# Performance work log

Hardware: AMD Instinct MI355X
Metric: run time of the kernel (lower is better)

## Reference

```python
import jax, jax.numpy as jnp
import numpy as np

B, N, S, C1, C2 = 8, 8192, 2048, 128, 256
H1, H2 = 256, 256
EPS_LN = 1e-5


def _layernorm_c(x, g, b):
    # LayerNorm over channel dim of [B, C, N]
    mu = jnp.mean(x, axis=1, keepdims=True)
    var = jnp.mean((x - mu) ** 2, axis=1, keepdims=True)
    return g[None, :, None] * (x - mu) / jnp.sqrt(var + EPS_LN) + b[None, :, None]


def setup_inputs() -> dict:
    key = jax.random.key(0)
    ks = jax.random.split(key, 8)
    Cin = C1 + C2
    return {
        "points_coor1": jax.random.normal(ks[0], (B, 3, N), jnp.float32),
        "points_coor2": jax.random.normal(ks[1], (B, 3, S), jnp.float32),
        "points_fea1": jax.random.normal(ks[2], (B, C1, N), jnp.float32),
        "points_fea2": jax.random.normal(ks[3], (B, C2, S), jnp.float32),
        "points_padding2": jnp.zeros((B, S), dtype=bool),
        "W1": jax.random.normal(ks[4], (H1, Cin), jnp.float32) * 0.05,
        "b1": jnp.zeros((H1,), jnp.float32),
        "g1": jnp.ones((H1,), jnp.float32),
        "be1": jnp.zeros((H1,), jnp.float32),
        "W2": jax.random.normal(ks[5], (H2, H1), jnp.float32) * 0.05,
        "b2": jnp.zeros((H2,), jnp.float32),
        "g2": jnp.ones((H2,), jnp.float32),
        "be2": jnp.zeros((H2,), jnp.float32),
    }


def reference(points_coor1, points_coor2, points_fea1, points_fea2,
              points_padding2, W1, b1, g1, be1, W2, b2, g2, be2):
    c1 = jnp.transpose(points_coor1, (0, 2, 1))  # [B,N,3]
    c2 = jnp.transpose(points_coor2, (0, 2, 1))  # [B,S,3]
    f2 = jnp.transpose(points_fea2, (0, 2, 1))   # [B,S,C2]

    # push padded points far away (max computed on unmodified coords, as in torch RHS-first eval)
    big = jnp.max(jnp.abs(c2)) * 3.0
    c2 = jnp.where(points_padding2[..., None], big, c2)

    # squared euclidean pairwise distances [B,N,S]
    d = (jnp.sum(c1 * c1, -1)[:, :, None]
         + jnp.sum(c2 * c2, -1)[:, None, :]
         - 2.0 * jnp.einsum('bnd,bsd->bns', c1, c2))

    neg_d, idx = jax.lax.top_k(-d, 3)          # 3 smallest distances
    dists = -neg_d                              # [B,N,3]
    recip = 1.0 / jnp.clip(dists, 1e-8)
    w = recip / jnp.sum(recip, axis=-1, keepdims=True)  # [B,N,3]

    gathered = jax.vmap(lambda f, i: f[i])(f2, idx)     # [B,N,3,C2]
    interp = jnp.einsum('bnkc,bnk->bcn', gathered, w)   # [B,C2,N]

    x = jnp.concatenate([points_fea1, interp], axis=1)  # [B,C1+C2,N]
    x = jax.nn.relu(_layernorm_c(jnp.einsum('oc,bcn->bon', W1, x) + b1[None, :, None], g1, be1))
    x = jax.nn.relu(_layernorm_c(jnp.einsum('oc,bcn->bon', W2, x) + b2[None, :, None], g2, be2))
    return x
```

## Files before the change

### kernel.cpp

```cpp
#include <hip/hip_runtime.h>
#include <stdint.h>

#define BB 8
#define NPT 8192
#define SPT 2048
#define C1D 128
#define C2D 256
#define CIN 384
#define HD 256
#define SPLIT 8
#define SC (SPT/SPLIT)

typedef __attribute__((ext_vector_type(8))) short bf16x8;
typedef __attribute__((ext_vector_type(4))) float f32x4;

__device__ __forceinline__ unsigned short f2b(float f){
  unsigned int u = __float_as_uint(f);
  u += 0x7fffu + ((u >> 16) & 1u);
  return (unsigned short)(u >> 16);
}

__global__ __launch_bounds__(256) void cvt_bf16_kernel(const float* __restrict__ src,
                                                       unsigned short* __restrict__ dst, int n){
  int i = blockIdx.x * 256 + threadIdx.x;
  if (i < n) dst[i] = f2b(src[i]);
}

__global__ __launch_bounds__(256) void gsrc_kernel(const float* __restrict__ coor2,
    const unsigned char* __restrict__ pad, float4* __restrict__ gs){
  int i = blockIdx.x * 256 + threadIdx.x;
  int b = i >> 11, s = i & (SPT - 1);
  const float* cb = coor2 + b * 3 * SPT;
  float x = cb[s], y = cb[SPT + s], z = cb[2*SPT + s];
  if (pad[i]) { x = 1e19f; y = 1e19f; z = 1e19f; }
  float n2 = __fadd_rn(__fadd_rn(__fmul_rn(x,x), __fmul_rn(y,y)), __fmul_rn(z,z));
  gs[i] = make_float4(x, y, z, n2);
}

__global__ __launch_bounds__(256) void transpose_cn(const float* __restrict__ src,
    unsigned short* __restrict__ dst, int Cdim, int Ndim, int dstStride){
  __shared__ unsigned short t[32][33];
  int b = blockIdx.z;
  int n0 = blockIdx.x * 32, c0 = blockIdx.y * 32;
  int tx = threadIdx.x, ty = threadIdx.y;
  const float* s = src + (size_t)b * Cdim * Ndim;
  unsigned short* d = dst + (size_t)b * Ndim * dstStride;
  #pragma unroll
  for (int i = 0; i < 4; i++)
    t[ty + i*8][tx] = f2b(s[(size_t)(c0 + ty + i*8) * Ndim + n0 + tx]);
  __syncthreads();
  #pragma unroll
  for (int i = 0; i < 4; i++)
    d[(size_t)(n0 + ty + i*8) * dstStride + c0 + tx] = t[tx][ty + i*8];
}

__global__ __launch_bounds__(256) void knn_part_kernel(const float* __restrict__ coor1,
    const float4* __restrict__ gs, float* __restrict__ cv, int* __restrict__ cj){
  int b = blockIdx.y, c = blockIdx.z;
  int s0c = c * SC;
  const float4* gsb = gs + b * SPT + s0c;
  int n = blockIdx.x * 256 + threadIdx.x;
  const float* ca = coor1 + b * 3 * NPT;
  float x1 = ca[n], y1 = ca[NPT + n], z1 = ca[2*NPT + n];
  float n1 = __fadd_rn(__fadd_rn(__fmul_rn(x1,x1), __fmul_rn(y1,y1)), __fmul_rn(z1,z1));
  float v0 = 3.4e38f, v1 = 3.4e38f, v2 = 3.4e38f;
  int j0 = 0, j1 = 0, j2 = 0;
  #pragma unroll 8
  for (int s = 0; s < SC; s++){
    float4 q = gsb[s];
    float dot = __fadd_rn(__fadd_rn(__fmul_rn(x1,q.x), __fmul_rn(y1,q.y)), __fmul_rn(z1,q.z));
    float npn = __fadd_rn(n1, q.w);
    float d = __builtin_fmaf(-2.0f, dot, npn);
    bool l0 = d < v0, l1 = d < v1, l2 = d < v2;
    j2 = l1 ? j1 : (l2 ? s : j2);
    j1 = l0 ? j0 : (l1 ? s : j1);
    j0 = l0 ? s  : j0;
    float nv2 = __builtin_amdgcn_fmed3f(v1, v2, d);
    float nv1 = __builtin_amdgcn_fmed3f(v0, v1, d);
    v0 = fminf(v0, d); v1 = nv1; v2 = nv2;
  }
  size_t m = (size_t)b * NPT + n;
  size_t base = (m * SPLIT + c) * 3;
  cv[base+0] = v0; cv[base+1] = v1; cv[base+2] = v2;
  cj[base+0] = s0c + j0; cj[base+1] = s0c + j1; cj[base+2] = s0c + j2;
}

__global__ __launch_bounds__(256) void knn_merge_kernel(const float* __restrict__ cv,
    const int* __restrict__ cj, float* __restrict__ w3, int* __restrict__ i3){
  size_t m = (size_t)blockIdx.x * 256 + threadIdx.x;
  float v0 = 3.4e38f, v1 = 3.4e38f, v2 = 3.4e38f;
  int j0 = 0, j1 = 0, j2 = 0;
  #pragma unroll
  for (int c = 0; c < SPLIT; c++){
    #pragma unroll
    for (int k = 0; k < 3; k++){
      float d = cv[(m * SPLIT + c) * 3 + k];
      int j   = cj[(m * SPLIT + c) * 3 + k];
      bool l0 = d < v0, l1 = d < v1, l2 = d < v2;
      j2 = l1 ? j1 : (l2 ? j : j2);
      j1 = l0 ? j0 : (l1 ? j : j1);
      j0 = l0 ? j  : j0;
      float nv2 = __builtin_amdgcn_fmed3f(v1, v2, d);
      float nv1 = __builtin_amdgcn_fmed3f(v0, v1, d);
      v0 = fminf(v0, d); v1 = nv1; v2 = nv2;
    }
  }
  float r0 = 1.0f / fmaxf(v0, 1e-8f);
  float r1 = 1.0f / fmaxf(v1, 1e-8f);
  float r2 = 1.0f / fmaxf(v2, 1e-8f);
  float rs = (r0 + r1) + r2;
  w3[m*3+0] = r0 / rs; w3[m*3+1] = r1 / rs; w3[m*3+2] = r2 / rs;
  i3[m*3+0] = j0; i3[m*3+1] = j1; i3[m*3+2] = j2;
}

__global__ __launch_bounds__(256) void interp_kernel(const unsigned short* __restrict__ f2t,
    const float* __restrict__ w3, const int* __restrict__ i3, unsigned short* __restrict__ xpm){
  int m = blockIdx.x * 4 + (threadIdx.x >> 6);
  int lane = threadIdx.x & 63;
  int b = m >> 13;
  int s0 = i3[m*3+0], s1 = i3[m*3+1], s2 = i3[m*3+2];
  float w0 = w3[m*3+0], w1 = w3[m*3+1], w2 = w3[m*3+2];
  const ushort4 a = *(const ushort4*)(f2t + (size_t)(b*SPT + s0) * C2D + lane*4);
  const ushort4 c = *(const ushort4*)(f2t + (size_t)(b*SPT + s1) * C2D + lane*4);
  const ushort4 e = *(const ushort4*)(f2t + (size_t)(b*SPT + s2) * C2D + lane*4);
  #define B2F(u) __uint_as_float(((unsigned int)(u)) << 16)
  ushort4 o;
  o.x = f2b(w0*B2F(a.x) + w1*B2F(c.x) + w2*B2F(e.x));
  o.y = f2b(w0*B2F(a.y) + w1*B2F(c.y) + w2*B2F(e.y));
  o.z = f2b(w0*B2F(a.z) + w1*B2F(c.z) + w2*B2F(e.z));
  o.w = f2b(w0*B2F(a.w) + w1*B2F(c.w) + w2*B2F(e.w));
  *(ushort4*)(xpm + (size_t)m * CIN + C1D + lane*4) = o;
}

__global__ __launch_bounds__(256) void mlp1_kernel(const unsigned short* __restrict__ xpm,
    const unsigned short* __restrict__ Wg, const float* __restrict__ bg,
    const float* __restrict__ gg, const float* __restrict__ beg,
    unsigned short* __restrict__ Hg){
  __shared__ __align__(16) unsigned short Ws[256*40];
  __shared__ __align__(16) unsigned short Xs[64*40];
  __shared__ __align__(16) unsigned short Hb[64*136];
  __shared__ float sB[256], sG[256], sBe[256];
  int tid = threadIdx.x;
  int m0 = blockIdx.x * 64;
  sB[tid] = bg[tid]; sG[tid] = gg[tid]; sBe[tid] = beg[tid];
  int w = tid >> 6, lane = tid & 63, col = lane & 15, quad = lane >> 4;
  f32x4 acc[16];
  #pragma unroll
  for (int i = 0; i < 16; i++) acc[i] = (f32x4)0.0f;
  for (int kb = 0; kb < CIN; kb += 32){
    __syncthreads();
    {
      const int4* s4 = (const int4*)(Wg + (size_t)tid * CIN + kb);
      int4* d4 = (int4*)(Ws + tid * 40);
      #pragma unroll
      for (int i = 0; i < 4; i++) d4[i] = s4[i];
    }
    {
      int mr = tid >> 2, part = tid & 3;
      *(int4*)(Xs + mr*40 + part*8) = *(const int4*)(xpm + (size_t)(m0 + mr) * CIN + kb + part*8);
    }
    __syncthreads();
    bf16x8 bfrag = *(const bf16x8*)(Xs + (w*16 + col)*40 + quad*8);
    #pragma unroll
    for (int ot = 0; ot < 16; ot++){
      bf16x8 afrag = *(const bf16x8*)(Ws + (ot*16 + col)*40 + quad*8);
      acc[ot] = __builtin_amdgcn_mfma_f32_16x16x32_bf16(afrag, bfrag, acc[ot], 0, 0, 0);
    }
  }
  float s1 = 0.f, s2 = 0.f;
  #pragma unroll
  for (int ot = 0; ot < 16; ot++)
    #pragma unroll
    for (int r = 0; r < 4; r++){
      int o = ot*16 + quad*4 + r;
      float v = acc[ot][r] + sB[o];
      acc[ot][r] = v;
      s1 += v; s2 += v*v;
    }
  s1 += __shfl_xor(s1, 16); s1 += __shfl_xor(s1, 32);
  s2 += __shfl_xor(s2, 16); s2 += __shfl_xor(s2, 32);
  float mu = s1 * (1.f/256.f);
  float rinv = rsqrtf(s2 * (1.f/256.f) - mu*mu + 1e-5f);
  for (int half = 0; half < 2; half++){
    __syncthreads();
    #pragma unroll
    for (int ot8 = 0; ot8 < 8; ot8++){
      int ot = half*8 + ot8;
      int ob = ot*16 + quad*4;
      ushort4 hv;
      hv.x = f2b(fmaxf((acc[ot][0] - mu) * rinv * sG[ob+0] + sBe[ob+0], 0.f));
      hv.y = f2b(fmaxf((acc[ot][1] - mu) * rinv * sG[ob+1] + sBe[ob+1], 0.f));
      hv.z = f2b(fmaxf((acc[ot][2] - mu) * rinv * sG[ob+2] + sBe[ob+2], 0.f));
      hv.w = f2b(fmaxf((acc[ot][3] - mu) * rinv * sG[ob+3] + sBe[ob+3], 0.f));
      *(ushort4*)(Hb + (w*16 + col)*136 + ot8*16 + quad*4) = hv;
    }
    __syncthreads();
    int mr = tid >> 2, part = tid & 3;
    #pragma unroll
    for (int r = 0; r < 4; r++){
      int piece = part*4 + r;
      *(int4*)(Hg + (size_t)(m0 + mr)*HD + half*128 + piece*8) = *(const int4*)(Hb + mr*136 + piece*8);
    }
  }
}

__global__ __launch_bounds__(256) void mlp2_kernel(const unsigned short* __restrict__ Hg,
    const unsigned short* __restrict__ Wg, const float* __restrict__ bg,
    const float* __restrict__ gg, const float* __restrict__ beg,
    float* __restrict__ outg){
  __shared__ __align__(16) unsigned short Ws[256*40];
  __shared__ __align__(16) unsigned short Xs[64*40];
  __shared__ float sB[256], sG[256], sBe[256];
  int tid = threadIdx.x;
  int m0 = blockIdx.x * 64;
  int b = m0 >> 13, n0 = m0 & (NPT - 1);
  sB[tid] = bg[tid]; sG[tid] = gg[tid]; sBe[tid] = beg[tid];
  int w = tid >> 6, lane = tid & 63, col = lane & 15, quad = lane >> 4;
  f32x4 acc[16];
  #pragma unroll
  for (int i = 0; i < 16; i++) acc[i] = (f32x4)0.0f;
  for (int kb = 0; kb < HD; kb += 32){
    __syncthreads();
    {
      const int4* s4 = (const int4*)(Wg + (size_t)tid * HD + kb);
      int4* d4 = (int4*)(Ws + tid * 40);
      #pragma unroll
      for (int i = 0; i < 4; i++) d4[i] = s4[i];
    }
    {
      int mr = tid >> 2, part = tid & 3;
      *(int4*)(Xs + mr*40 + part*8) = *(const int4*)(Hg + (size_t)(m0 + mr) * HD + kb + part*8);
    }
    __syncthreads();
    bf16x8 bfrag = *(const bf16x8*)(Xs + (w*16 + col)*40 + quad*8);
    #pragma unroll
    for (int ot = 0; ot < 16; ot++){
      bf16x8 afrag = *(const bf16x8*)(Ws + (ot*16 + col)*40 + quad*8);
      acc[ot] = __builtin_amdgcn_mfma_f32_16x16x32_bf16(afrag, bfrag, acc[ot], 0, 0, 0);
    }
  }
  float s1 = 0.f, s2 = 0.f;
  #pragma unroll
  for (int ot = 0; ot < 16; ot++)
    #pragma unroll
    for (int r = 0; r < 4; r++){
      int o = ot*16 + quad*4 + r;
      float v = acc[ot][r] + sB[o];
      acc[ot][r] = v;
      s1 += v; s2 += v*v;
    }
  s1 += __shfl_xor(s1, 16); s1 += __shfl_xor(s1, 32);
  s2 += __shfl_xor(s2, 16); s2 += __shfl_xor(s2, 32);
  float mu = s1 * (1.f/256.f);
  float rinv = rsqrtf(s2 * (1.f/256.f) - mu*mu + 1e-5f);
  size_t obase = (size_t)b * HD * NPT + n0 + w*16 + col;
  #pragma unroll
  for (int ot = 0; ot < 16; ot++)
    #pragma unroll
    for (int r = 0; r < 4; r++){
      int o = ot*16 + quad*4 + r;
      float v = (acc[ot][r] - mu) * rinv * sG[o] + sBe[o];
      outg[obase + (size_t)o * NPT] = fmaxf(v, 0.f);
    }
}

extern "C" void kernel_launch(void* const* d_in, const int* in_sizes, int n_in,
                              void* d_out, int out_size, void* d_ws, size_t ws_size,
                              hipStream_t stream){
  const float* coor1 = (const float*)d_in[0];
  const float* coor2 = (const float*)d_in[1];
  const float* fea1  = (const float*)d_in[2];
  const float* fea2  = (const float*)d_in[3];
  const unsigned char* pad = (const unsigned char*)d_in[4];
  const float* W1  = (const float*)d_in[5];
  const float* b1  = (const float*)d_in[6];
  const float* g1  = (const float*)d_in[7];
  const float* be1 = (const float*)d_in[8];
  const float* W2  = (const float*)d_in[9];
  const float* b2  = (const float*)d_in[10];
  const float* g2  = (const float*)d_in[11];
  const float* be2 = (const float*)d_in[12];
  float* out = (float*)d_out;

  char* ws = (char*)d_ws;
  float* w3            = (float*)(ws + 256);
  int*   i3            = (int*)  (ws + 786688);
  unsigned short* W1b  = (unsigned short*)(ws + 1573120);
  unsigned short* W2b  = (unsigned short*)(ws + 1769728);
  unsigned short* f2t  = (unsigned short*)(ws + 1900800);
  unsigned short* xpm  = (unsigned short*)(ws + 10289408);
  unsigned short* Hg   = (unsigned short*)(ws + 60621056);
  float* cv            = (float*)(ws + 60621056);
  int*   cj            = (int*)  (ws + 60621056 + 6291456);
  float4* gs           = (float4*)(ws + 60621056 + 16777216);

  cvt_bf16_kernel<<<(HD*CIN + 255)/256, 256, 0, stream>>>(W1, W1b, HD*CIN);
  cvt_bf16_kernel<<<(HD*HD + 255)/256, 256, 0, stream>>>(W2, W2b, HD*HD);
  gsrc_kernel<<<BB*SPT/256, 256, 0, stream>>>(coor2, pad, gs);
  dim3 tb(32, 8);
  transpose_cn<<<dim3(SPT/32, C2D/32, BB), tb, 0, stream>>>(fea2, f2t, C2D, SPT, C2D);
  transpose_cn<<<dim3(NPT/32, C1D/32, BB), tb, 0, stream>>>(fea1, xpm, C1D, NPT, CIN);
  knn_part_kernel<<<dim3(NPT/256, BB, SPLIT), 256, 0, stream>>>(coor1, gs, cv, cj);
  knn_merge_kernel<<<BB*NPT/256, 256, 0, stream>>>(cv, cj, w3, i3);
  interp_kernel<<<BB*NPT/4, 256, 0, stream>>>(f2t, w3, i3, xpm);
  mlp1_kernel<<<BB*NPT/64, 256, 0, stream>>>(xpm, W1b, b1, g1, be1, Hg);
  mlp2_kernel<<<BB*NPT/64, 256, 0, stream>>>(Hg, W2b, b2, g2, be2, out);
}
```

Baseline: 287.8 us.

## Double-buffer weight tiles and prefetch activations in MLP GEMM kernels

Both MLP kernels now prefetch the next K-chunk of weights into registers and write it to a second LDS buffer while MFMAs run on the current one, cutting barriers to one per iteration. Activation fragments are loaded directly from global memory into registers rather than staged through shared memory. The two weight-to-bf16 conversion kernels are merged into one launch. This costs more LDS and registers, which may reduce occupancy.

```diff
diff --git a/kernel.cpp b/kernel.cpp
--- a/kernel.cpp
+++ b/kernel.cpp
@@ -20,10 +20,15 @@
   return (unsigned short)(u >> 16);
 }
 
-__global__ __launch_bounds__(256) void cvt_bf16_kernel(const float* __restrict__ src,
-                                                       unsigned short* __restrict__ dst, int n){
+__global__ __launch_bounds__(256) void cvt2_bf16_kernel(const float* __restrict__ W1,
+    const float* __restrict__ W2, unsigned short* __restrict__ dst){
   int i = blockIdx.x * 256 + threadIdx.x;
-  if (i < n) dst[i] = f2b(src[i]);
+  const int n1 = HD * CIN;
+  if (i < n1) dst[i] = f2b(W1[i]);
+  else {
+    int k = i - n1;
+    if (k < HD * HD) dst[n1 + k] = f2b(W2[k]);
+  }
 }
 
 __global__ __launch_bounds__(256) void gsrc_kernel(const float* __restrict__ coor2,
@@ -136,36 +141,48 @@
     const unsigned short* __restrict__ Wg, const float* __restrict__ bg,
     const float* __restrict__ gg, const float* __restrict__ beg,
     unsigned short* __restrict__ Hg){
-  __shared__ __align__(16) unsigned short Ws[256*40];
-  __shared__ __align__(16) unsigned short Xs[64*40];
+  __shared__ __align__(16) unsigned short Ws[2][256*40];
   __shared__ __align__(16) unsigned short Hb[64*136];
   __shared__ float sB[256], sG[256], sBe[256];
   int tid = threadIdx.x;
   int m0 = blockIdx.x * 64;
   sB[tid] = bg[tid]; sG[tid] = gg[tid]; sBe[tid] = beg[tid];
   int w = tid >> 6, lane = tid & 63, col = lane & 15, quad = lane >> 4;
+  const unsigned short* xrow = xpm + (size_t)(m0 + w*16 + col) * CIN + quad*8;
+  const int4* wsrc = (const int4*)(Wg + (size_t)tid * CIN);
+  bf16x8 xnext = *(const bf16x8*)(xrow);
+  {
+    int4* d4 = (int4*)(&Ws[0][tid * 40]);
+    #pragma unroll
+    for (int i = 0; i < 4; i++) d4[i] = wsrc[i];
+  }
   f32x4 acc[16];
   #pragma unroll
   for (int i = 0; i < 16; i++) acc[i] = (f32x4)0.0f;
-  for (int kb = 0; kb < CIN; kb += 32){
+  __syncthreads();
+  #pragma unroll 2
+  for (int c = 0; c < 12; c++){
+    int4 wreg[4];
+    bf16x8 xn2;
+    if (c + 1 < 12){
+      #pragma unroll
+      for (int i = 0; i < 4; i++) wreg[i] = wsrc[(c+1)*4 + i];
+      xn2 = *(const bf16x8*)(xrow + (c+1)*32);
+    }
+    bf16x8 bfrag = xnext;
+    const unsigned short* wsbase = &Ws[c & 1][0];
+    #pragma unroll
+    for (int ot = 0; ot < 16; ot++){
+      bf16x8 afrag = *(const bf16x8*)(wsbase + (ot*16 + col)*40 + quad*8);
+      acc[ot] = __builtin_amdgcn_mfma_f32_16x16x32_bf16(afrag, bfrag, acc[ot], 0, 0, 0);
+    }
+    if (c + 1 < 12){
+      int4* d4 = (int4*)(&Ws[(c+1) & 1][tid * 40]);
+      #pragma unroll
+      for (int i = 0; i < 4; i++) d4[i] = wreg[i];
+      xnext = xn2;
+    }
     __syncthreads();
-    {
-      const int4* s4 = (const int4*)(Wg + (size_t)tid * CIN + kb);
-      int4* d4 = (int4*)(Ws + tid * 40);
-      #pragma unroll
-      for (int i = 0; i < 4; i++) d4[i] = s4[i];
-    }
-    {
-      int mr = tid >> 2, part = tid & 3;
-      *(int4*)(Xs + mr*40 + part*8) = *(const int4*)(xpm + (size_t)(m0 + mr) * CIN + kb + part*8);
-    }
-    __syncthreads();
-    bf16x8 bfrag = *(const bf16x8*)(Xs + (w*16 + col)*40 + quad*8);
-    #pragma unroll
-    for (int ot = 0; ot < 16; ot++){
-      bf16x8 afrag = *(const bf16x8*)(Ws + (ot*16 + col)*40 + quad*8);
-      acc[ot] = __builtin_amdgcn_mfma_f32_16x16x32_bf16(afrag, bfrag, acc[ot], 0, 0, 0);
-    }
   }
   float s1 = 0.f, s2 = 0.f;
   #pragma unroll
@@ -208,36 +225,48 @@
     const unsigned short* __restrict__ Wg, const float* __restrict__ bg,
     const float* __restrict__ gg, const float* __restrict__ beg,
     float* __restrict__ outg){
-  __shared__ __align__(16) unsigned short Ws[256*40];
-  __shared__ __align__(16) unsigned short Xs[64*40];
+  __shared__ __align__(16) unsigned short Ws[2][256*40];
   __shared__ float sB[256], sG[256], sBe[256];
   int tid = threadIdx.x;
   int m0 = blockIdx.x * 64;
   int b = m0 >> 13, n0 = m0 & (NPT - 1);
   sB[tid] = bg[tid]; sG[tid] = gg[tid]; sBe[tid] = beg[tid];
   int w = tid >> 6, lane = tid & 63, col = lane & 15, quad = lane >> 4;
+  const unsigned short* xrow = Hg + (size_t)(m0 + w*16 + col) * HD + quad*8;
+  const int4* wsrc = (const int4*)(Wg + (size_t)tid * HD);
+  bf16x8 xnext = *(const bf16x8*)(xrow);
+  {
+    int4* d4 = (int4*)(&Ws[0][tid * 40]);
+    #pragma unroll
+    for (int i = 0; i < 4; i++) d4[i] = wsrc[i];
+  }
   f32x4 acc[16];
   #pragma unroll
   for (int i = 0; i < 16; i++) acc[i] = (f32x4)0.0f;
-  for (int kb = 0; kb < HD; kb += 32){
+  __syncthreads();
+  #pragma unroll 2
+  for (int c = 0; c < 8; c++){
+    int4 wreg[4];
+    bf16x8 xn2;
+    if (c + 1 < 8){
+      #pragma unroll
+      for (int i = 0; i < 4; i++) wreg[i] = wsrc[(c+1)*4 + i];
+      xn2 = *(const bf16x8*)(xrow + (c+1)*32);
+    }
+    bf16x8 bfrag = xnext;
+    const unsigned short* wsbase = &Ws[c & 1][0];
+    #pragma unroll
+    for (int ot = 0; ot < 16; ot++){
+      bf16x8 afrag = *(const bf16x8*)(wsbase + (ot*16 + col)*40 + quad*8);
+      acc[ot] = __builtin_amdgcn_mfma_f32_16x16x32_bf16(afrag, bfrag, acc[ot], 0, 0, 0);
+    }
+    if (c + 1 < 8){
+      int4* d4 = (int4*)(&Ws[(c+1) & 1][tid * 40]);
+      #pragma unroll
+      for (int i = 0; i < 4; i++) d4[i] = wreg[i];
+      xnext = xn2;
+    }
     __syncthreads();
-    {
-      const int4* s4 = (const int4*)(Wg + (size_t)tid * HD + kb);
-      int4* d4 = (int4*)(Ws + tid * 40);
-      #pragma unroll
-      for (int i = 0; i < 4; i++) d4[i] = s4[i];
-    }
-    {
-      int mr = tid >> 2, part = tid & 3;
-      *(int4*)(Xs + mr*40 + part*8) = *(const int4*)(Hg + (size_t)(m0 + mr) * HD + kb + part*8);
-    }
-    __syncthreads();
-    bf16x8 bfrag = *(const bf16x8*)(Xs + (w*16 + col)*40 + quad*8);
-    #pragma unroll
-    for (int ot = 0; ot < 16; ot++){
-      bf16x8 afrag = *(const bf16x8*)(Ws + (ot*16 + col)*40 + quad*8);
-      acc[ot] = __builtin_amdgcn_mfma_f32_16x16x32_bf16(afrag, bfrag, acc[ot], 0, 0, 0);
-    }
   }
   float s1 = 0.f, s2 = 0.f;
   #pragma unroll
@@ -294,8 +323,7 @@
   int*   cj            = (int*)  (ws + 60621056 + 6291456);
   float4* gs           = (float4*)(ws + 60621056 + 16777216);
 
-  cvt_bf16_kernel<<<(HD*CIN + 255)/256, 256, 0, stream>>>(W1, W1b, HD*CIN);
-  cvt_bf16_kernel<<<(HD*HD + 255)/256, 256, 0, stream>>>(W2, W2b, HD*HD);
+  cvt2_bf16_kernel<<<(HD*CIN + HD*HD + 255)/256, 256, 0, stream>>>(W1, W2, W1b);
   gsrc_kernel<<<BB*SPT/256, 256, 0, stream>>>(coor2, pad, gs);
   dim3 tb(32, 8);
   transpose_cn<<<dim3(SPT/32, C2D/32, BB), tb, 0, stream>>>(fea2, f2t, C2D, SPT, C2D);
```

New measurement: 322.7 us. +12.1%, slower.
